# Kernel optimization log

Hardware: AMD Instinct MI355X
Metric: run time of the kernel (lower is better)

## Reference

```python
import jax, jax.numpy as jnp
import numpy as np

DN = ('NCHW', 'OIHW', 'NCHW')

def dw_conv(x, w, pad):
    # depthwise conv, w: [C,1,k,k], groups=C
    return jax.lax.conv_general_dilated(x, w, (1, 1), [(pad, pad), (pad, pad)],
                                         dimension_numbers=DN, feature_group_count=x.shape[1])

def pw_conv(x, w):
    # 1x1 pointwise conv, w: [Cout,Cin,1,1]
    return jax.lax.conv_general_dilated(x, w, (1, 1), 'VALID', dimension_numbers=DN)

def hardswish(x):
    return x * jnp.clip(x + 3.0, 0.0, 6.0) * (1.0 / 6.0)

def batchnorm(x, g, b, m, v, eps=1e-5):
    scale = (g / jnp.sqrt(v + eps))[None, :, None, None]
    return (x - m[None, :, None, None]) * scale + b[None, :, None, None]

def layernorm(x, g, b, eps=1e-5):
    mu = x.mean(-1, keepdims=True)
    var = x.var(-1, keepdims=True)
    return (x - mu) / jnp.sqrt(var + eps) * g + b

def setup_inputs() -> dict:
    key = jax.random.key(0)
    ks = jax.random.split(key, 16)
    B, C, H, W = 8, 256, 64, 64
    sd = 64   # seg_dim
    s = 0.05  # weight init scale
    inp = {
        'x':   jax.random.normal(ks[0], (B, C, H, W), jnp.float32),
        'seg': jax.random.normal(ks[1], (B, C, H, W), jnp.float32),
        'kv_w':   jax.random.normal(ks[2], (2 * C, C), jnp.float32) * s,
        'q_w':    jax.random.normal(ks[3], (C, C), jnp.float32) * s,
        'proj_w': jax.random.normal(ks[4], (C, C), jnp.float32) * s,
        'proj_b': jnp.zeros((C,), jnp.float32),
        'agg0_dw': jax.random.normal(ks[5], (3 * sd, 1, 3, 3), jnp.float32) * s,
        'agg0_pw': jax.random.normal(ks[6], (sd, 3 * sd, 1, 1), jnp.float32) * s,
        'ln_g': jnp.ones((sd,), jnp.float32), 'ln_b': jnp.zeros((sd,), jnp.float32),
        'agg1_dw': jax.random.normal(ks[7], (sd, 1, 3, 3), jnp.float32) * s,
        'agg1_pw': jax.random.normal(ks[8], (sd, sd, 1, 1), jnp.float32) * s,
        'bn1_g': jnp.ones((sd,), jnp.float32), 'bn1_b': jnp.zeros((sd,), jnp.float32),
        'bn1_m': jnp.zeros((sd,), jnp.float32), 'bn1_v': jnp.ones((sd,), jnp.float32),
        'agg2_dw': jax.random.normal(ks[9], (sd, 1, 5, 5), jnp.float32) * s,
        'agg2_pw': jax.random.normal(ks[10], (sd, sd, 1, 1), jnp.float32) * s,
        'bn2_g': jnp.ones((sd,), jnp.float32), 'bn2_b': jnp.zeros((sd,), jnp.float32),
        'bn2_m': jnp.zeros((sd,), jnp.float32), 'bn2_v': jnp.ones((sd,), jnp.float32),
        'agg3_dw': jax.random.normal(ks[11], (sd, 1, 7, 7), jnp.float32) * s,
        'agg3_pw': jax.random.normal(ks[12], (sd, sd, 1, 1), jnp.float32) * s,
        'bn3_g': jnp.ones((sd,), jnp.float32), 'bn3_b': jnp.zeros((sd,), jnp.float32),
        'bn3_m': jnp.zeros((sd,), jnp.float32), 'bn3_v': jnp.ones((sd,), jnp.float32),
        'crpe_w3': jax.random.normal(ks[13], (48, 1, 3, 3), jnp.float32) * s,
        'crpe_b3': jnp.zeros((48,), jnp.float32),
        'crpe_w5': jax.random.normal(ks[14], (72, 1, 5, 5), jnp.float32) * s,
        'crpe_b5': jnp.zeros((72,), jnp.float32),
        'crpe_w7': jax.random.normal(ks[15], (72, 1, 7, 7), jnp.float32) * s,
        'crpe_b7': jnp.zeros((72,), jnp.float32),
    }
    return inp

def reference(x, seg, kv_w, q_w, proj_w, proj_b, agg0_dw, agg0_pw, ln_g, ln_b,
              agg1_dw, agg1_pw, bn1_g, bn1_b, bn1_m, bn1_v,
              agg2_dw, agg2_pw, bn2_g, bn2_b, bn2_m, bn2_v,
              agg3_dw, agg3_pw, bn3_g, bn3_b, bn3_m, bn3_v,
              crpe_w3, crpe_b3, crpe_w5, crpe_b5, crpe_w7, crpe_b7):
    B, C, H, W = x.shape
    N = H * W
    num_heads = 8
    scale = (C // num_heads) ** -0.5  # head_dim = 32 -> 32^-0.5
    sd = C // 4                       # seg_dim = 64
    Ct = C // 4 * 3                   # trans_dim = 192
    Ch = Ct // num_heads              # 24

    # NOTE: faithful to torch: plain reshape of [B,C,H,W] -> [B,N,C] (no transpose)
    xf = x.reshape(B, N, C)
    sf = seg.reshape(B, N, C)

    kv = (xf @ kv_w.T).reshape(B, N, 2, C)
    kv = jnp.transpose(kv, (2, 0, 1, 3)).reshape(2 * B, N, C)
    q = sf @ q_w.T                                  # [B,N,C]
    qkv = jnp.concatenate([q, kv], axis=0)          # [3B,N,C]

    # ---- Aggregator ----
    xa = jnp.transpose(qkv, (0, 2, 1)).reshape(3 * B, C, H, W)
    c0, c1, c2, c3 = (xa[:, :sd], xa[:, sd:2 * sd], xa[:, 2 * sd:3 * sd], xa[:, 3 * sd:])
    # agg0 branch (local): regroup q/k/v copies into channels
    xl = c3.reshape(3, B, sd, H, W)
    xl = jnp.transpose(xl, (1, 0, 2, 3, 4)).reshape(B, 3 * sd, H, W)
    xl = pw_conv(dw_conv(xl, agg0_dw, 1), agg0_pw)  # [B,sd,H,W]
    xl = jnp.transpose(xl.reshape(B, sd, N), (0, 2, 1))
    x_agg0 = hardswish(layernorm(xl, ln_g, ln_b))   # [B,N,sd]

    x1 = hardswish(batchnorm(pw_conv(dw_conv(c0, agg1_dw, 1), agg1_pw), bn1_g, bn1_b, bn1_m, bn1_v))
    x2 = hardswish(batchnorm(pw_conv(dw_conv(c1, agg2_dw, 2), agg2_pw), bn2_g, bn2_b, bn2_m, bn2_v))
    x3 = hardswish(batchnorm(pw_conv(dw_conv(c2, agg3_dw, 3), agg3_pw), bn3_g, bn3_b, bn3_m, bn3_v))
    xc = jnp.concatenate([x1, x2, x3], axis=1)       # [3B,Ct,H,W]
    qkv_t = xc.reshape(3, B, num_heads, Ch, N)
    qkv_t = jnp.transpose(qkv_t, (0, 1, 2, 4, 3))    # [3,B,h,N,Ch]
    qh, kh, vh = qkv_t[0], qkv_t[1], qkv_t[2]

    # ---- linear attention: softmax over tokens on k, then k^T v ----
    k_sm = jax.nn.softmax(kh, axis=2)                       # softmax over N
    ktv = jnp.einsum('bhnk,bhnv->bhkv', k_sm, vh)           # [B,h,Ch,Ch]
    eff_att = jnp.einsum('bhnk,bhkv->bhnv', qh, ktv)        # [B,h,N,Ch]

    # ---- ConvRelPosEnc ----
    v_img = jnp.transpose(vh, (0, 1, 3, 2)).reshape(B, num_heads * Ch, H, W)
    s1, s2 = 2 * Ch, 2 * Ch + 3 * Ch   # channel splits [48,72,72]
    cv3 = dw_conv(v_img[:, :s1], crpe_w3, 1) + crpe_b3[None, :, None, None]
    cv5 = dw_conv(v_img[:, s1:s2], crpe_w5, 2) + crpe_b5[None, :, None, None]
    cv7 = dw_conv(v_img[:, s2:], crpe_w7, 3) + crpe_b7[None, :, None, None]
    conv_v = jnp.concatenate([cv3, cv5, cv7], axis=1)
    conv_v = jnp.transpose(conv_v.reshape(B, num_heads, Ch, N), (0, 1, 3, 2))  # [B,h,N,Ch]
    crpe = qh * conv_v

    out = scale * eff_att + crpe                     # [B,h,N,Ch]
    out = jnp.transpose(out, (0, 2, 1, 3)).reshape(B, N, Ct)
    out = jnp.concatenate([out, x_agg0], axis=-1)    # [B,N,C]
    out = out @ proj_w.T + proj_b
    return out
```

## Files before the change

### kernel.cpp

```cpp
#include <hip/hip_runtime.h>
#include <math.h>

#define DI __device__ __forceinline__

typedef unsigned short u16;
typedef __attribute__((ext_vector_type(8))) short bf16x8;
typedef __attribute__((ext_vector_type(4))) float f32x4;

static constexpr int Cc = 256;
static constexpr int Nn = 4096;

DI float hswish(float v) { return v * fminf(fmaxf(v + 3.f, 0.f), 6.f) * (1.f / 6.f); }

DI u16 f2b(float f) {
  union { float f; unsigned int u; } c; c.f = f;
  return (u16)((c.u + 0x7FFFu + ((c.u >> 16) & 1u)) >> 16);
}

typedef const __attribute__((address_space(1))) unsigned int* gas1_t;
typedef __attribute__((address_space(3))) unsigned int* las3_t;
DI void gld16(const void* g, void* l) {
  __builtin_amdgcn_global_load_lds((gas1_t)g, (las3_t)l, 16, 0, 0);
}

__global__ __launch_bounds__(256) void k_cvt(
    const float4* __restrict__ x, const float4* __restrict__ seg,
    const float4* __restrict__ kvw, const float4* __restrict__ qw,
    const float4* __restrict__ pw,
    ushort4* __restrict__ xb, ushort4* __restrict__ segb,
    ushort4* __restrict__ kvwb, ushort4* __restrict__ qwb,
    ushort4* __restrict__ pwb)
{
  const int total = 4259840;
  for (int i = blockIdx.x * 256 + threadIdx.x; i < total; i += gridDim.x * 256) {
    const float4* s; ushort4* d; int j;
    if (i < 2097152)      { s = x;   d = xb;   j = i; }
    else if (i < 4194304) { s = seg; d = segb; j = i - 2097152; }
    else if (i < 4227072) { s = kvw; d = kvwb; j = i - 4194304; }
    else if (i < 4243456) { s = qw;  d = qwb;  j = i - 4227072; }
    else                  { s = pw;  d = pwb;  j = i - 4243456; }
    float4 v = s[j];
    ushort4 o;
    o.x = f2b(v.x); o.y = f2b(v.y); o.z = f2b(v.z); o.w = f2b(v.w);
    d[j] = o;
  }
}

__global__ __launch_bounds__(256) void k_qkv(
    const u16* __restrict__ xb, const u16* __restrict__ segb,
    const u16* __restrict__ kvwb, const u16* __restrict__ qwb,
    float* __restrict__ qkv)
{
  __shared__ __align__(16) u16 As[2][4096];
  __shared__ __align__(16) u16 Bs[2][4096];
  const int t = threadIdx.x;
  const int lane = t & 63, wave = t >> 6;
  const int n0 = blockIdx.x * 128;
  const int c0 = blockIdx.y * 128;
  const int g  = blockIdx.z;
  const int grp = g >> 3, b = g & 7;
  const u16* __restrict__ In = (grp == 0 ? segb : xb) + (size_t)b * Nn * Cc;
  const u16* __restrict__ Wg = (grp == 0) ? qwb : (kvwb + (grp == 2 ? Cc * Cc : 0));

  const int rA = lane & 15;
  const int kA = (lane >> 4) * 8;
  const int s0 = wave * 2, s1 = wave * 2 + 1;

#define STAGE(buf, k0)                                                        \
  {                                                                           \
    gld16(Wg + (size_t)(c0 + s0 * 16 + rA) * Cc + (k0) + kA, &As[buf][s0 * 512]); \
    gld16(In + (size_t)(n0 + s0 * 16 + rA) * Cc + (k0) + kA, &Bs[buf][s0 * 512]); \
    gld16(Wg + (size_t)(c0 + s1 * 16 + rA) * Cc + (k0) + kA, &As[buf][s1 * 512]); \
    gld16(In + (size_t)(n0 + s1 * 16 + rA) * Cc + (k0) + kA, &Bs[buf][s1 * 512]); \
  }

  f32x4 acc[4][4];
#pragma unroll
  for (int m = 0; m < 4; ++m)
#pragma unroll
    for (int n = 0; n < 4; ++n) acc[m][n] = (f32x4){0.f, 0.f, 0.f, 0.f};

  const int asub = (wave >> 1) * 4;
  const int bsub = (wave & 1) * 4;

  STAGE(0, 0);
  for (int ks = 0; ks < 8; ++ks) {
    __syncthreads();
    if (ks < 7) STAGE((ks + 1) & 1, (ks + 1) * 32);
    const int cur = ks & 1;
    bf16x8 af[4], bfr[4];
#pragma unroll
    for (int m = 0; m < 4; ++m)
      af[m] = *(const bf16x8*)&As[cur][(asub + m) * 512 + lane * 8];
#pragma unroll
    for (int n = 0; n < 4; ++n)
      bfr[n] = *(const bf16x8*)&Bs[cur][(bsub + n) * 512 + lane * 8];
#pragma unroll
    for (int m = 0; m < 4; ++m)
#pragma unroll
      for (int n = 0; n < 4; ++n)
        acc[m][n] = __builtin_amdgcn_mfma_f32_16x16x32_bf16(af[m], bfr[n], acc[m][n], 0, 0, 0);
  }
#undef STAGE

  const int wc = (wave >> 1) * 64, wn = (wave & 1) * 64;
  const int row4 = (lane >> 4) * 4, col = lane & 15;
  float* __restrict__ op = qkv + (size_t)(g * Cc + c0 + wc) * Nn + n0 + wn;
#pragma unroll
  for (int m = 0; m < 4; ++m)
#pragma unroll
    for (int nn = 0; nn < 4; ++nn)
#pragma unroll
      for (int r = 0; r < 4; ++r)
        op[(size_t)(m * 16 + row4 + r) * Nn + nn * 16 + col] = acc[m][nn][r];
}

template <int KS>
DI void dw_plane(const float* __restrict__ sp, const float* __restrict__ wl,
                 float* __restrict__ dst, float bias, int t)
{
  constexpr int P = KS / 2;
  float wr[KS * KS];
#pragma unroll
  for (int i = 0; i < KS * KS; ++i) wr[i] = wl[i];
  const int x = t & 63;
  const int yb = (t >> 6) << 4;
  float acc[16];
#pragma unroll
  for (int i = 0; i < 16; ++i) acc[i] = bias;
#pragma unroll
  for (int r = 0; r < 16 + 2 * P; ++r) {
    float v[KS];
    const float* rp = sp + (yb + r + (3 - P)) * 70 + x + (3 - P);
#pragma unroll
    for (int dx = 0; dx < KS; ++dx) v[dx] = rp[dx];
#pragma unroll
    for (int dy = 0; dy < KS; ++dy) {
      const int yl = r - dy;
      if (yl >= 0 && yl < 16) {
        float s = acc[yl];
#pragma unroll
        for (int dx = 0; dx < KS; ++dx) s += wr[dy * KS + dx] * v[dx];
        acc[yl] = s;
      }
    }
  }
#pragma unroll
  for (int yl = 0; yl < 16; ++yl) dst[(yb + yl) * 64 + x] = acc[yl];
}

__global__ __launch_bounds__(256) void k_dw(
    const float* __restrict__ qkv,
    const float* __restrict__ a1w, const float* __restrict__ a2w,
    const float* __restrict__ a3w, const float* __restrict__ a0w,
    float* __restrict__ dwout, float* __restrict__ dwout0)
{
  __shared__ float sp[70 * 70];
  __shared__ float wl[49];
  const int t = threadIdx.x;
  const int p = blockIdx.x;
  const float* src; float* dst; const float* wsp; int ks;
  if (p < 4608) {
    int g = p / 192, c = p % 192, r = c >> 6;
    ks = 3 + 2 * r;
    wsp = (r == 0 ? a1w : (r == 1 ? a2w : a3w)) + (c & 63) * ks * ks;
    src = qkv + (size_t)(g * 256 + c) * Nn;
    dst = dwout + (size_t)p * Nn;
  } else {
    int q = p - 4608;
    int b = q / 192, j = q % 192;
    ks = 3;
    wsp = a0w + j * 9;
    src = qkv + (size_t)(((j >> 6) * 8 + b) * 256 + 192 + (j & 63)) * Nn;
    dst = dwout0 + (size_t)q * Nn;
  }
  for (int i = t; i < 4900; i += 256) sp[i] = 0.f;
  if (t < 49) wl[t] = (t < ks * ks) ? wsp[t] : 0.f;
  __syncthreads();
#pragma unroll
  for (int i = 0; i < 16; ++i) {
    int e = t + i * 256;
    sp[((e >> 6) + 3) * 70 + (e & 63) + 3] = src[e];
  }
  __syncthreads();
  if (ks == 3)      dw_plane<3>(sp, wl, dst, 0.f, t);
  else if (ks == 5) dw_plane<5>(sp, wl, dst, 0.f, t);
  else              dw_plane<7>(sp, wl, dst, 0.f, t);
}

__global__ __launch_bounds__(256) void k_crpe(
    const float* __restrict__ xc,
    const float* __restrict__ w3, const float* __restrict__ b3,
    const float* __restrict__ w5, const float* __restrict__ b5,
    const float* __restrict__ w7, const float* __restrict__ b7,
    float* __restrict__ conv_v)
{
  __shared__ float sp[70 * 70];
  __shared__ float wl[49];
  const int t = threadIdx.x;
  const int p = blockIdx.x;
  const int b = p / 192, ch = p % 192;
  const float* wsp; float bias; int ks;
  if (ch < 48)       { ks = 3; wsp = w3 + ch * 9;          bias = b3[ch]; }
  else if (ch < 120) { ks = 5; wsp = w5 + (ch - 48) * 25;  bias = b5[ch - 48]; }
  else               { ks = 7; wsp = w7 + (ch - 120) * 49; bias = b7[ch - 120]; }
  const float* src = xc + (size_t)((16 + b) * 192 + ch) * Nn;
  float* dst = conv_v + (size_t)p * Nn;
  for (int i = t; i < 4900; i += 256) sp[i] = 0.f;
  if (t < 49) wl[t] = (t < ks * ks) ? wsp[t] : 0.f;
  __syncthreads();
#pragma unroll
  for (int i = 0; i < 16; ++i) {
    int e = t + i * 256;
    sp[((e >> 6) + 3) * 70 + (e & 63) + 3] = src[e];
  }
  __syncthreads();
  if (ks == 3)      dw_plane<3>(sp, wl, dst, bias, t);
  else if (ks == 5) dw_plane<5>(sp, wl, dst, bias, t);
  else              dw_plane<7>(sp, wl, dst, bias, t);
}

__global__ __launch_bounds__(256) void k_pw_bn(
    const float* __restrict__ dwout,
    const float* __restrict__ w1, const float* __restrict__ w2, const float* __restrict__ w3,
    const float* __restrict__ g1, const float* __restrict__ be1, const float* __restrict__ m1, const float* __restrict__ v1,
    const float* __restrict__ g2, const float* __restrict__ be2, const float* __restrict__ m2, const float* __restrict__ v2,
    const float* __restrict__ g3, const float* __restrict__ be3, const float* __restrict__ m3, const float* __restrict__ v3,
    float* __restrict__ xc)
{
  __shared__ float Tl[64][128];
  __shared__ float Wt[64][64];
  const int t = threadIdx.x;
  const int n0 = blockIdx.x * 128;
  const int r = blockIdx.y;
  const int g = blockIdx.z;
  const float* Wp = (r == 0 ? w1 : (r == 1 ? w2 : w3));
  const float* bg = (r == 0 ? g1 : (r == 1 ? g2 : g3));
  const float* bb = (r == 0 ? be1 : (r == 1 ? be2 : be3));
  const float* bm = (r == 0 ? m1 : (r == 1 ? m2 : m3));
  const float* bv = (r == 0 ? v1 : (r == 1 ? v2 : v3));
  const size_t ibase = (size_t)(g * 192 + r * 64) * Nn + n0;
#pragma unroll
  for (int i = 0; i < 8; ++i) {
    int e = t + i * 256;
    int ci = e >> 5, nf = (e & 31) * 4;
    *(float4*)&Tl[ci][nf] = *(const float4*)(dwout + ibase + (size_t)ci * Nn + nf);
  }
#pragma unroll
  for (int i = 0; i < 16; ++i) {
    int e = t + i * 256;
    int co = e & 63, ci = e >> 6;
    Wt[ci][co] = Wp[co * 64 + ci];
  }
  __syncthreads();
  const int tn = (t & 15) * 4;
  const int tc = (t >> 4) * 4;
  float acc[4][8];
#pragma unroll
  for (int i = 0; i < 4; ++i)
#pragma unroll
    for (int j = 0; j < 8; ++j) acc[i][j] = 0.f;
#pragma unroll 8
  for (int ci = 0; ci < 64; ++ci) {
    const float4 i0 = *(const float4*)&Tl[ci][tn];
    const float4 i1 = *(const float4*)&Tl[ci][64 + tn];
    const float4 wv = *(const float4*)&Wt[ci][tc];
    const float iv[8] = {i0.x, i0.y, i0.z, i0.w, i1.x, i1.y, i1.z, i1.w};
    const float wa[4] = {wv.x, wv.y, wv.z, wv.w};
#pragma unroll
    for (int i = 0; i < 4; ++i)
#pragma unroll
      for (int j = 0; j < 8; ++j) acc[i][j] += wa[i] * iv[j];
  }
  const size_t obase = (size_t)(g * 192 + r * 64 + tc) * Nn + n0;
#pragma unroll
  for (int i = 0; i < 4; ++i) {
    int co = tc + i;
    float sc = bg[co] * rsqrtf(bv[co] + 1e-5f);
    float sh = bb[co] - bm[co] * sc;
    float4 o0, o1;
    o0.x = hswish(acc[i][0] * sc + sh); o0.y = hswish(acc[i][1] * sc + sh);
    o0.z = hswish(acc[i][2] * sc + sh); o0.w = hswish(acc[i][3] * sc + sh);
    o1.x = hswish(acc[i][4] * sc + sh); o1.y = hswish(acc[i][5] * sc + sh);
    o1.z = hswish(acc[i][6] * sc + sh); o1.w = hswish(acc[i][7] * sc + sh);
    *(float4*)(xc + obase + (size_t)i * Nn + tn) = o0;
    *(float4*)(xc + obase + (size_t)i * Nn + 64 + tn) = o1;
  }
}

__global__ __launch_bounds__(256) void k_pw_ln(
    const float* __restrict__ dwout0, const float* __restrict__ pw,
    const float* __restrict__ lng, const float* __restrict__ lnb,
    float* __restrict__ x_agg0)
{
  __shared__ float Tl[64][128];
  __shared__ float Wt[64][64];
  const int t = threadIdx.x;
  const int n0 = blockIdx.x * 128;
  const int b = blockIdx.y;
  const int tn = (t & 15) * 4;
  const int tc = (t >> 4) * 4;
  float acc[4][8];
#pragma unroll
  for (int i = 0; i < 4; ++i)
#pragma unroll
    for (int j = 0; j < 8; ++j) acc[i][j] = 0.f;

  for (int kc = 0; kc < 192; kc += 64) {
#pragma unroll
    for (int i = 0; i < 8; ++i) {
      int e = t + i * 256;
      int ci = e >> 5, nf = (e & 31) * 4;
      *(float4*)&Tl[ci][nf] =
          *(const float4*)(dwout0 + (size_t)(b * 192 + kc + ci) * Nn + n0 + nf);
    }
#pragma unroll
    for (int i = 0; i < 16; ++i) {
      int e = t + i * 256;
      int co = e & 63, ci = e >> 6;
      Wt[ci][co] = pw[co * 192 + kc + ci];
    }
    __syncthreads();
#pragma unroll 8
    for (int ci = 0; ci < 64; ++ci) {
      const float4 i0 = *(const float4*)&Tl[ci][tn];
      const float4 i1 = *(const float4*)&Tl[ci][64 + tn];
      const float4 wv = *(const float4*)&Wt[ci][tc];
      const float iv[8] = {i0.x, i0.y, i0.z, i0.w, i1.x, i1.y, i1.z, i1.w};
      const float wa[4] = {wv.x, wv.y, wv.z, wv.w};
#pragma unroll
      for (int i = 0; i < 4; ++i)
#pragma unroll
        for (int j = 0; j < 8; ++j) acc[i][j] += wa[i] * iv[j];
    }
    __syncthreads();
  }
  float* redS = &Tl[0][0];
  float* redQ = &Tl[0][0] + 2048;
  float* muA = &Tl[0][0] + 4096;
  float* isA = &Tl[0][0] + 4224;
#pragma unroll
  for (int j = 0; j < 8; ++j) {
    int nl = (j < 4) ? (tn + j) : (64 + tn + j - 4);
    float s = acc[0][j] + acc[1][j] + acc[2][j] + acc[3][j];
    float q = acc[0][j] * acc[0][j] + acc[1][j] * acc[1][j] +
              acc[2][j] * acc[2][j] + acc[3][j] * acc[3][j];
    redS[(t >> 4) * 128 + nl] = s;
    redQ[(t >> 4) * 128 + nl] = q;
  }
  __syncthreads();
  if (t < 128) {
    float s = 0.f, q = 0.f;
#pragma unroll
    for (int rr = 0; rr < 16; ++rr) { s += redS[rr * 128 + t]; q += redQ[rr * 128 + t]; }
    float mu = s * (1.f / 64.f);
    float var = q * (1.f / 64.f) - mu * mu;
    muA[t] = mu;
    isA[t] = rsqrtf(var + 1e-5f);
  }
  __syncthreads();
  float lg[4], lb[4];
#pragma unroll
  for (int i = 0; i < 4; ++i) { lg[i] = lng[tc + i]; lb[i] = lnb[tc + i]; }
#pragma unroll
  for (int j = 0; j < 8; ++j) {
    int nl = (j < 4) ? (tn + j) : (64 + tn + j - 4);
    float mu = muA[nl], is = isA[nl];
    float4 o;
    o.x = hswish((acc[0][j] - mu) * is * lg[0] + lb[0]);
    o.y = hswish((acc[1][j] - mu) * is * lg[1] + lb[1]);
    o.z = hswish((acc[2][j] - mu) * is * lg[2] + lb[2]);
    o.w = hswish((acc[3][j] - mu) * is * lg[3] + lb[3]);
    *(float4*)(x_agg0 + (size_t)((b << 12) + n0 + nl) * 64 + tc) = o;
  }
}

__global__ __launch_bounds__(256) void k_sm(const float* __restrict__ xc,
                                            float* __restrict__ ls)
{
  __shared__ float rA[4], rB[4];
  const int rho = blockIdx.x;
  const int b = rho / 192, rem = rho % 192;
  const float* row = xc + (size_t)((8 + b) * 192 + rem) * Nn;
  const int t = threadIdx.x;
  float v[16];
#pragma unroll
  for (int i = 0; i < 16; ++i) v[i] = row[t + i * 256];
  float m = v[0];
#pragma unroll
  for (int i = 1; i < 16; ++i) m = fmaxf(m, v[i]);
#pragma unroll
  for (int off = 32; off > 0; off >>= 1) m = fmaxf(m, __shfl_xor(m, off, 64));
  if ((t & 63) == 0) rA[t >> 6] = m;
  __syncthreads();
  m = fmaxf(fmaxf(rA[0], rA[1]), fmaxf(rA[2], rA[3]));
  float s = 0.f;
#pragma unroll
  for (int i = 0; i < 16; ++i) s += __expf(v[i] - m);
#pragma unroll
  for (int off = 32; off > 0; off >>= 1) s += __shfl_xor(s, off, 64);
  if ((t & 63) == 0) rB[t >> 6] = s;
  __syncthreads();
  if (t == 0) ls[rho] = m + __logf(rB[0] + rB[1] + rB[2] + rB[3]);
}

__global__ __launch_bounds__(576) void k_ktv(const float* __restrict__ xc,
                                             const float* __restrict__ ls,
                                             float* __restrict__ ktv)
{
  __shared__ float pb[24][65];
  __shared__ float vb[24][65];
  __shared__ float lsl[24];
  const int nc = blockIdx.x, h = blockIdx.y, b = blockIdx.z;
  const int t = threadIdx.x;
  if (t < 24) lsl[t] = ls[(b * 8 + h) * 24 + t];
  __syncthreads();
  const int kk = t / 24, vv = t % 24;
  const float* kbase = xc + (size_t)((8 + b) * 192 + h * 24) * Nn;
  const float* vbase = xc + (size_t)((16 + b) * 192 + h * 24) * Nn;
  const int nb0 = nc * 512;
  float accv = 0.f;
  for (int sub = 0; sub < 8; ++sub) {
    int nbase = nb0 + sub * 64;
    for (int e = t; e < 1536; e += 576) {
      int ch = e >> 6, n = e & 63;
      pb[ch][n] = __expf(kbase[(size_t)ch * Nn + nbase + n] - lsl[ch]);
      vb[ch][n] = vbase[(size_t)ch * Nn + nbase + n];
    }
    __syncthreads();
    float a = 0.f;
#pragma unroll 16
    for (int i = 0; i < 64; ++i) a += pb[kk][i] * vb[vv][i];
    accv += a;
    __syncthreads();
  }
  atomicAdd(&ktv[((b * 8 + h) * 24 + kk) * 24 + vv], accv);
}

__global__ __launch_bounds__(256) void k_cat(
    const float* __restrict__ xc, const float* __restrict__ conv_v,
    const float* __restrict__ ktv, const float* __restrict__ x_agg0,
    u16* __restrict__ catb)
{
  __shared__ float kt[4608];
  const int t = threadIdx.x;
  const int b = blockIdx.y;
  for (int e = t; e < 4608; e += 256) kt[e] = ktv[b * 4608 + e];
  __syncthreads();
  const int nl = t & 63;
  const int grp = t >> 6;
  const int n = blockIdx.x * 64 + nl;
  const float scale = 0.17677669529663687f;
#pragma unroll
  for (int hh = 0; hh < 2; ++hh) {
    const int h = grp * 2 + hh;
    const float* qb = xc + (size_t)(b * 192 + h * 24) * Nn + n;
    float q[24];
#pragma unroll
    for (int c = 0; c < 24; ++c) q[c] = qb[(size_t)c * Nn];
    float ev[24];
#pragma unroll
    for (int v = 0; v < 24; ++v) ev[v] = 0.f;
    const float* kth = kt + h * 576;
#pragma unroll
    for (int k = 0; k < 24; ++k) {
      const float qk = q[k];
#pragma unroll
      for (int v = 0; v < 24; ++v) ev[v] += qk * kth[k * 24 + v];
    }
    const float* cvb = conv_v + (size_t)(b * 192 + h * 24) * Nn + n;
    u16* ob = catb + ((size_t)(b * 4096 + n)) * 256 + h * 24;
#pragma unroll
    for (int v4 = 0; v4 < 6; ++v4) {
      ushort4 o;
      o.x = f2b(scale * ev[v4 * 4 + 0] + q[v4 * 4 + 0] * cvb[(size_t)(v4 * 4 + 0) * Nn]);
      o.y = f2b(scale * ev[v4 * 4 + 1] + q[v4 * 4 + 1] * cvb[(size_t)(v4 * 4 + 1) * Nn]);
      o.z = f2b(scale * ev[v4 * 4 + 2] + q[v4 * 4 + 2] * cvb[(size_t)(v4 * 4 + 2) * Nn]);
      o.w = f2b(scale * ev[v4 * 4 + 3] + q[v4 * 4 + 3] * cvb[(size_t)(v4 * 4 + 3) * Nn]);
      *(ushort4*)(ob + v4 * 4) = o;
    }
  }
  const float* xa = x_agg0 + ((size_t)(b * 4096 + blockIdx.x * 64)) * 64;
  u16* cb = catb + ((size_t)(b * 4096 + blockIdx.x * 64)) * 256 + 192;
  for (int e2 = t; e2 < 4096; e2 += 256) {
    int nn = e2 >> 6, cc = e2 & 63;
    cb[(size_t)nn * 256 + cc] = f2b(xa[(size_t)nn * 64 + cc]);
  }
}

__global__ __launch_bounds__(256) void k_proj(
    const u16* __restrict__ catb, const u16* __restrict__ pwb,
    const float* __restrict__ pb, float* __restrict__ out)
{
  __shared__ __align__(16) u16 As[2][4096];
  __shared__ __align__(16) u16 Bs[2][4096];
  const int t = threadIdx.x;
  const int lane = t & 63, wave = t >> 6;
  const int m0 = blockIdx.x * 128;
  const int c0 = blockIdx.y * 128;
  const int rA = lane & 15;
  const int kA = (lane >> 4) * 8;
  const int s0 = wave * 2, s1 = wave * 2 + 1;

#define STAGE(buf, k0)                                                        \
  {                                                                           \
    gld16(catb + (size_t)(m0 + s0 * 16 + rA) * 256 + (k0) + kA, &As[buf][s0 * 512]); \
    gld16(pwb  + (size_t)(c0 + s0 * 16 + rA) * 256 + (k0) + kA, &Bs[buf][s0 * 512]); \
    gld16(catb + (size_t)(m0 + s1 * 16 + rA) * 256 + (k0) + kA, &As[buf][s1 * 512]); \
    gld16(pwb  + (size_t)(c0 + s1 * 16 + rA) * 256 + (k0) + kA, &Bs[buf][s1 * 512]); \
  }

  f32x4 acc[4][4];
#pragma unroll
  for (int m = 0; m < 4; ++m)
#pragma unroll
    for (int n = 0; n < 4; ++n) acc[m][n] = (f32x4){0.f, 0.f, 0.f, 0.f};

  const int asub = (wave >> 1) * 4;
  const int bsub = (wave & 1) * 4;

  STAGE(0, 0);
  for (int ks = 0; ks < 8; ++ks) {
    __syncthreads();
    if (ks < 7) STAGE((ks + 1) & 1, (ks + 1) * 32);
    const int cur = ks & 1;
    bf16x8 af[4], bfr[4];
#pragma unroll
    for (int m = 0; m < 4; ++m)
      af[m] = *(const bf16x8*)&As[cur][(asub + m) * 512 + lane * 8];
#pragma unroll
    for (int n = 0; n < 4; ++n)
      bfr[n] = *(const bf16x8*)&Bs[cur][(bsub + n) * 512 + lane * 8];
#pragma unroll
    for (int m = 0; m < 4; ++m)
#pragma unroll
      for (int n = 0; n < 4; ++n)
        acc[m][n] = __builtin_amdgcn_mfma_f32_16x16x32_bf16(af[m], bfr[n], acc[m][n], 0, 0, 0);
  }
#undef STAGE

  const int wm = (wave >> 1) * 64, wn = (wave & 1) * 64;
  const int row4 = (lane >> 4) * 4, col = lane & 15;
  float pbv[4];
#pragma unroll
  for (int nn = 0; nn < 4; ++nn) pbv[nn] = pb[c0 + wn + nn * 16 + col];
  float* __restrict__ op = out + (size_t)(m0 + wm) * 256 + c0 + wn;
#pragma unroll
  for (int mi = 0; mi < 4; ++mi)
#pragma unroll
    for (int nn = 0; nn < 4; ++nn)
#pragma unroll
      for (int r = 0; r < 4; ++r)
        op[(size_t)(mi * 16 + row4 + r) * 256 + nn * 16 + col] = acc[mi][nn][r] + pbv[nn];
}

extern "C" void kernel_launch(void* const* d_in, const int* in_sizes, int n_in,
                              void* d_out, int out_size, void* d_ws, size_t ws_size,
                              hipStream_t stream)
{
  const float* x       = (const float*)d_in[0];
  const float* seg     = (const float*)d_in[1];
  const float* kv_w    = (const float*)d_in[2];
  const float* q_w     = (const float*)d_in[3];
  const float* proj_w  = (const float*)d_in[4];
  const float* proj_b  = (const float*)d_in[5];
  const float* agg0_dw = (const float*)d_in[6];
  const float* agg0_pw = (const float*)d_in[7];
  const float* ln_g    = (const float*)d_in[8];
  const float* ln_b    = (const float*)d_in[9];
  const float* agg1_dw = (const float*)d_in[10];
  const float* agg1_pw = (const float*)d_in[11];
  const float* bn1_g   = (const float*)d_in[12];
  const float* bn1_b   = (const float*)d_in[13];
  const float* bn1_m   = (const float*)d_in[14];
  const float* bn1_v   = (const float*)d_in[15];
  const float* agg2_dw = (const float*)d_in[16];
  const float* agg2_pw = (const float*)d_in[17];
  const float* bn2_g   = (const float*)d_in[18];
  const float* bn2_b   = (const float*)d_in[19];
  const float* bn2_m   = (const float*)d_in[20];
  const float* bn2_v   = (const float*)d_in[21];
  const float* agg3_dw = (const float*)d_in[22];
  const float* agg3_pw = (const float*)d_in[23];
  const float* bn3_g   = (const float*)d_in[24];
  const float* bn3_b   = (const float*)d_in[25];
  const float* bn3_m   = (const float*)d_in[26];
  const float* bn3_v   = (const float*)d_in[27];
  const float* crpe_w3 = (const float*)d_in[28];
  const float* crpe_b3 = (const float*)d_in[29];
  const float* crpe_w5 = (const float*)d_in[30];
  const float* crpe_b5 = (const float*)d_in[31];
  const float* crpe_w7 = (const float*)d_in[32];
  const float* crpe_b7 = (const float*)d_in[33];

  float* ws = (float*)d_ws;
  float* qkv    = ws;
  float* xcbuf  = ws;
  float* dwout  = ws + 25165824;
  float* conv_v = dwout;
  u16*   xb     = (u16*)(ws + 25165824);
  u16*   segb   = (u16*)(ws + 29360128);
  u16*   kvwb   = (u16*)(ws + 33554432);
  u16*   qwb    = (u16*)(ws + 33619968);
  float* dwout0 = ws + 44040192;
  u16*   catb   = (u16*)(ws + 44040192);
  float* x_agg0 = ws + 50331648;
  float* ls     = ws + 52428800;
  float* ktv    = ws + 52430336;
  u16*   pwb    = (u16*)(ws + 52467200);
  float* out    = (float*)d_out;

  hipMemsetAsync(ktv, 0, 36864 * sizeof(float), stream);

  k_cvt<<<dim3(1024), 256, 0, stream>>>(
      (const float4*)x, (const float4*)seg, (const float4*)kv_w,
      (const float4*)q_w, (const float4*)proj_w,
      (ushort4*)xb, (ushort4*)segb, (ushort4*)kvwb, (ushort4*)qwb, (ushort4*)pwb);
  k_qkv<<<dim3(32, 2, 24), 256, 0, stream>>>(xb, segb, kvwb, qwb, qkv);
  k_dw<<<dim3(6144), 256, 0, stream>>>(qkv, agg1_dw, agg2_dw, agg3_dw, agg0_dw,
                                       dwout, dwout0);
  k_pw_bn<<<dim3(32, 3, 24), 256, 0, stream>>>(
      dwout, agg1_pw, agg2_pw, agg3_pw,
      bn1_g, bn1_b, bn1_m, bn1_v,
      bn2_g, bn2_b, bn2_m, bn2_v,
      bn3_g, bn3_b, bn3_m, bn3_v, xcbuf);
  k_pw_ln<<<dim3(32, 8), 256, 0, stream>>>(dwout0, agg0_pw, ln_g, ln_b, x_agg0);
  k_sm<<<dim3(1536), 256, 0, stream>>>(xcbuf, ls);
  k_ktv<<<dim3(8, 8, 8), 576, 0, stream>>>(xcbuf, ls, ktv);
  k_crpe<<<dim3(1536), 256, 0, stream>>>(xcbuf, crpe_w3, crpe_b3, crpe_w5,
                                         crpe_b5, crpe_w7, crpe_b7, conv_v);
  k_cat<<<dim3(64, 8), 256, 0, stream>>>(xcbuf, conv_v, ktv, x_agg0, catb);
  k_proj<<<dim3(256, 2), 256, 0, stream>>>(catb, pwb, proj_b, out);
}
```

Baseline: 400.2 us.

## Store intermediates in bf16, fuse input conversion into GEMMs, use MFMA for pointwise convs

Removes the separate fp32-to-bf16 conversion kernel. The QKV and projection GEMMs now load fp32 inputs and convert them in registers before writing to LDS. All intermediate activations (qkv, depthwise outputs, xc, conv_v, x_agg0) are stored as bf16 instead of fp32, roughly halving intermediate memory traffic. The pointwise BN and LN convolutions switch from scalar FMA to bf16 MFMA, and depthwise staging zeroes only the halo with a padded stride. The cost is lower-precision intermediates and losing the async global_load_lds path for the converted operands.

```diff
diff --git a/kernel.cpp b/kernel.cpp
--- a/kernel.cpp
+++ b/kernel.cpp
@@ -1,10 +1,10 @@
 #include <hip/hip_runtime.h>
-#include <math.h>
 
 #define DI __device__ __forceinline__
 
 typedef unsigned short u16;
 typedef __attribute__((ext_vector_type(8))) short bf16x8;
+typedef __attribute__((ext_vector_type(8))) unsigned short u16x8;
 typedef __attribute__((ext_vector_type(4))) float f32x4;
 
 static constexpr int Cc = 256;
@@ -15,6 +15,15 @@
 DI u16 f2b(float f) {
   union { float f; unsigned int u; } c; c.f = f;
   return (u16)((c.u + 0x7FFFu + ((c.u >> 16) & 1u)) >> 16);
+}
+DI float b2f(u16 v) {
+  union { unsigned int u; float f; } c; c.u = ((unsigned int)v) << 16; return c.f;
+}
+DI u16x8 pack8(float4 a, float4 b) {
+  u16x8 r;
+  r[0] = f2b(a.x); r[1] = f2b(a.y); r[2] = f2b(a.z); r[3] = f2b(a.w);
+  r[4] = f2b(b.x); r[5] = f2b(b.y); r[6] = f2b(b.z); r[7] = f2b(b.w);
+  return r;
 }
 
 typedef const __attribute__((address_space(1))) unsigned int* gas1_t;
@@ -23,33 +32,10 @@
   __builtin_amdgcn_global_load_lds((gas1_t)g, (las3_t)l, 16, 0, 0);
 }
 
-__global__ __launch_bounds__(256) void k_cvt(
-    const float4* __restrict__ x, const float4* __restrict__ seg,
-    const float4* __restrict__ kvw, const float4* __restrict__ qw,
-    const float4* __restrict__ pw,
-    ushort4* __restrict__ xb, ushort4* __restrict__ segb,
-    ushort4* __restrict__ kvwb, ushort4* __restrict__ qwb,
-    ushort4* __restrict__ pwb)
-{
-  const int total = 4259840;
-  for (int i = blockIdx.x * 256 + threadIdx.x; i < total; i += gridDim.x * 256) {
-    const float4* s; ushort4* d; int j;
-    if (i < 2097152)      { s = x;   d = xb;   j = i; }
-    else if (i < 4194304) { s = seg; d = segb; j = i - 2097152; }
-    else if (i < 4227072) { s = kvw; d = kvwb; j = i - 4194304; }
-    else if (i < 4243456) { s = qw;  d = qwb;  j = i - 4227072; }
-    else                  { s = pw;  d = pwb;  j = i - 4243456; }
-    float4 v = s[j];
-    ushort4 o;
-    o.x = f2b(v.x); o.y = f2b(v.y); o.z = f2b(v.z); o.w = f2b(v.w);
-    d[j] = o;
-  }
-}
-
 __global__ __launch_bounds__(256) void k_qkv(
-    const u16* __restrict__ xb, const u16* __restrict__ segb,
-    const u16* __restrict__ kvwb, const u16* __restrict__ qwb,
-    float* __restrict__ qkv)
+    const float* __restrict__ x, const float* __restrict__ seg,
+    const float* __restrict__ kv_w, const float* __restrict__ q_w,
+    u16* __restrict__ qkv)
 {
   __shared__ __align__(16) u16 As[2][4096];
   __shared__ __align__(16) u16 Bs[2][4096];
@@ -59,19 +45,27 @@
   const int c0 = blockIdx.y * 128;
   const int g  = blockIdx.z;
   const int grp = g >> 3, b = g & 7;
-  const u16* __restrict__ In = (grp == 0 ? segb : xb) + (size_t)b * Nn * Cc;
-  const u16* __restrict__ Wg = (grp == 0) ? qwb : (kvwb + (grp == 2 ? Cc * Cc : 0));
+  const float* __restrict__ In = (grp == 0 ? seg : x) + (size_t)b * Nn * Cc;
+  const float* __restrict__ Wg = (grp == 0) ? q_w : (kv_w + (grp == 2 ? Cc * Cc : 0));
 
   const int rA = lane & 15;
   const int kA = (lane >> 4) * 8;
   const int s0 = wave * 2, s1 = wave * 2 + 1;
 
-#define STAGE(buf, k0)                                                        \
+#define STG(buf, k0)                                                          \
   {                                                                           \
-    gld16(Wg + (size_t)(c0 + s0 * 16 + rA) * Cc + (k0) + kA, &As[buf][s0 * 512]); \
-    gld16(In + (size_t)(n0 + s0 * 16 + rA) * Cc + (k0) + kA, &Bs[buf][s0 * 512]); \
-    gld16(Wg + (size_t)(c0 + s1 * 16 + rA) * Cc + (k0) + kA, &As[buf][s1 * 512]); \
-    gld16(In + (size_t)(n0 + s1 * 16 + rA) * Cc + (k0) + kA, &Bs[buf][s1 * 512]); \
+    const float* ap0 = Wg + (size_t)(c0 + s0 * 16 + rA) * Cc + (k0) + kA;     \
+    const float* ap1 = Wg + (size_t)(c0 + s1 * 16 + rA) * Cc + (k0) + kA;     \
+    const float* bp0 = In + (size_t)(n0 + s0 * 16 + rA) * Cc + (k0) + kA;     \
+    const float* bp1 = In + (size_t)(n0 + s1 * 16 + rA) * Cc + (k0) + kA;     \
+    float4 a0 = *(const float4*)ap0, a1 = *(const float4*)(ap0 + 4);          \
+    float4 a2 = *(const float4*)ap1, a3 = *(const float4*)(ap1 + 4);          \
+    float4 b0 = *(const float4*)bp0, b1 = *(const float4*)(bp0 + 4);          \
+    float4 b2 = *(const float4*)bp1, b3 = *(const float4*)(bp1 + 4);          \
+    *(u16x8*)&As[buf][s0 * 512 + lane * 8] = pack8(a0, a1);                   \
+    *(u16x8*)&As[buf][s1 * 512 + lane * 8] = pack8(a2, a3);                   \
+    *(u16x8*)&Bs[buf][s0 * 512 + lane * 8] = pack8(b0, b1);                   \
+    *(u16x8*)&Bs[buf][s1 * 512 + lane * 8] = pack8(b2, b3);                   \
   }
 
   f32x4 acc[4][4];
@@ -83,10 +77,10 @@
   const int asub = (wave >> 1) * 4;
   const int bsub = (wave & 1) * 4;
 
-  STAGE(0, 0);
+  STG(0, 0);
   for (int ks = 0; ks < 8; ++ks) {
     __syncthreads();
-    if (ks < 7) STAGE((ks + 1) & 1, (ks + 1) * 32);
+    if (ks < 7) STG((ks + 1) & 1, (ks + 1) * 32);
     const int cur = ks & 1;
     bf16x8 af[4], bfr[4];
 #pragma unroll
@@ -101,23 +95,23 @@
       for (int n = 0; n < 4; ++n)
         acc[m][n] = __builtin_amdgcn_mfma_f32_16x16x32_bf16(af[m], bfr[n], acc[m][n], 0, 0, 0);
   }
-#undef STAGE
+#undef STG
 
   const int wc = (wave >> 1) * 64, wn = (wave & 1) * 64;
   const int row4 = (lane >> 4) * 4, col = lane & 15;
-  float* __restrict__ op = qkv + (size_t)(g * Cc + c0 + wc) * Nn + n0 + wn;
+  u16* __restrict__ op = qkv + (size_t)(g * Cc + c0 + wc) * Nn + n0 + wn;
 #pragma unroll
   for (int m = 0; m < 4; ++m)
 #pragma unroll
     for (int nn = 0; nn < 4; ++nn)
 #pragma unroll
       for (int r = 0; r < 4; ++r)
-        op[(size_t)(m * 16 + row4 + r) * Nn + nn * 16 + col] = acc[m][nn][r];
+        op[(size_t)(m * 16 + row4 + r) * Nn + nn * 16 + col] = f2b(acc[m][nn][r]);
 }
 
 template <int KS>
 DI void dw_plane(const float* __restrict__ sp, const float* __restrict__ wl,
-                 float* __restrict__ dst, float bias, int t)
+                 u16* __restrict__ dst, float bias, int t)
 {
   constexpr int P = KS / 2;
   float wr[KS * KS];
@@ -131,7 +125,7 @@
 #pragma unroll
   for (int r = 0; r < 16 + 2 * P; ++r) {
     float v[KS];
-    const float* rp = sp + (yb + r + (3 - P)) * 70 + x + (3 - P);
+    const float* rp = sp + (yb + r + (3 - P)) * 72 + x + (4 - P);
 #pragma unroll
     for (int dx = 0; dx < KS; ++dx) v[dx] = rp[dx];
 #pragma unroll
@@ -146,20 +140,46 @@
     }
   }
 #pragma unroll
-  for (int yl = 0; yl < 16; ++yl) dst[(yb + yl) * 64 + x] = acc[yl];
+  for (int yl = 0; yl < 16; ++yl) dst[(yb + yl) * 64 + x] = f2b(acc[yl]);
+}
+
+DI void dw_stage(const u16* __restrict__ src, float* __restrict__ sp, int t)
+{
+  for (int i = t; i < 944; i += 256) {
+    if (i < 432) {
+      int r6 = i / 72, cl = i - r6 * 72;
+      int row = (r6 < 3) ? r6 : 64 + r6;
+      sp[row * 72 + cl] = 0.f;
+    } else {
+      int i2 = i - 432;
+      int row = 3 + (i2 >> 3), k = i2 & 7;
+      int cl = (k < 4) ? k : 64 + k;
+      sp[row * 72 + cl] = 0.f;
+    }
+  }
+#pragma unroll
+  for (int i = 0; i < 2; ++i) {
+    int u = t + i * 256;
+    int row = u >> 3, c8 = (u & 7) * 8;
+    u16x8 v = *(const u16x8*)(src + row * 64 + c8);
+    float4 f0 = make_float4(b2f(v[0]), b2f(v[1]), b2f(v[2]), b2f(v[3]));
+    float4 f1 = make_float4(b2f(v[4]), b2f(v[5]), b2f(v[6]), b2f(v[7]));
+    *(float4*)&sp[(row + 3) * 72 + 4 + c8] = f0;
+    *(float4*)&sp[(row + 3) * 72 + 8 + c8] = f1;
+  }
 }
 
 __global__ __launch_bounds__(256) void k_dw(
-    const float* __restrict__ qkv,
+    const u16* __restrict__ qkv,
     const float* __restrict__ a1w, const float* __restrict__ a2w,
     const float* __restrict__ a3w, const float* __restrict__ a0w,
-    float* __restrict__ dwout, float* __restrict__ dwout0)
-{
-  __shared__ float sp[70 * 70];
+    u16* __restrict__ dwout, u16* __restrict__ dwout0)
+{
+  __shared__ float sp[70 * 72];
   __shared__ float wl[49];
   const int t = threadIdx.x;
   const int p = blockIdx.x;
-  const float* src; float* dst; const float* wsp; int ks;
+  const u16* src; u16* dst; const float* wsp; int ks;
   if (p < 4608) {
     int g = p / 192, c = p % 192, r = c >> 6;
     ks = 3 + 2 * r;
@@ -174,14 +194,8 @@
     src = qkv + (size_t)(((j >> 6) * 8 + b) * 256 + 192 + (j & 63)) * Nn;
     dst = dwout0 + (size_t)q * Nn;
   }
-  for (int i = t; i < 4900; i += 256) sp[i] = 0.f;
   if (t < 49) wl[t] = (t < ks * ks) ? wsp[t] : 0.f;
-  __syncthreads();
-#pragma unroll
-  for (int i = 0; i < 16; ++i) {
-    int e = t + i * 256;
-    sp[((e >> 6) + 3) * 70 + (e & 63) + 3] = src[e];
-  }
+  dw_stage(src, sp, t);
   __syncthreads();
   if (ks == 3)      dw_plane<3>(sp, wl, dst, 0.f, t);
   else if (ks == 5) dw_plane<5>(sp, wl, dst, 0.f, t);
@@ -189,13 +203,13 @@
 }
 
 __global__ __launch_bounds__(256) void k_crpe(
-    const float* __restrict__ xc,
+    const u16* __restrict__ xc,
     const float* __restrict__ w3, const float* __restrict__ b3,
     const float* __restrict__ w5, const float* __restrict__ b5,
     const float* __restrict__ w7, const float* __restrict__ b7,
-    float* __restrict__ conv_v)
-{
-  __shared__ float sp[70 * 70];
+    u16* __restrict__ conv_v)
+{
+  __shared__ float sp[70 * 72];
   __shared__ float wl[49];
   const int t = threadIdx.x;
   const int p = blockIdx.x;
@@ -204,16 +218,10 @@
   if (ch < 48)       { ks = 3; wsp = w3 + ch * 9;          bias = b3[ch]; }
   else if (ch < 120) { ks = 5; wsp = w5 + (ch - 48) * 25;  bias = b5[ch - 48]; }
   else               { ks = 7; wsp = w7 + (ch - 120) * 49; bias = b7[ch - 120]; }
-  const float* src = xc + (size_t)((16 + b) * 192 + ch) * Nn;
-  float* dst = conv_v + (size_t)p * Nn;
-  for (int i = t; i < 4900; i += 256) sp[i] = 0.f;
+  const u16* src = xc + (size_t)((16 + b) * 192 + ch) * Nn;
+  u16* dst = conv_v + (size_t)p * Nn;
   if (t < 49) wl[t] = (t < ks * ks) ? wsp[t] : 0.f;
-  __syncthreads();
-#pragma unroll
-  for (int i = 0; i < 16; ++i) {
-    int e = t + i * 256;
-    sp[((e >> 6) + 3) * 70 + (e & 63) + 3] = src[e];
-  }
+  dw_stage(src, sp, t);
   __syncthreads();
   if (ks == 3)      dw_plane<3>(sp, wl, dst, bias, t);
   else if (ks == 5) dw_plane<5>(sp, wl, dst, bias, t);
@@ -221,16 +229,19 @@
 }
 
 __global__ __launch_bounds__(256) void k_pw_bn(
-    const float* __restrict__ dwout,
+    const u16* __restrict__ dwout,
     const float* __restrict__ w1, const float* __restrict__ w2, const float* __restrict__ w3,
     const float* __restrict__ g1, const float* __restrict__ be1, const float* __restrict__ m1, const float* __restrict__ v1,
     const float* __restrict__ g2, const float* __restrict__ be2, const float* __restrict__ m2, const float* __restrict__ v2,
     const float* __restrict__ g3, const float* __restrict__ be3, const float* __restrict__ m3, const float* __restrict__ v3,
-    float* __restrict__ xc)
-{
-  __shared__ float Tl[64][128];
-  __shared__ float Wt[64][64];
-  const int t = threadIdx.x;
+    u16* __restrict__ xc)
+{
+  constexpr int S2 = 134;
+  __shared__ u16 Dl[64 * S2];
+  __shared__ __align__(16) u16 Wt[64 * 72];
+  __shared__ float scA[64], shA[64];
+  const int t = threadIdx.x;
+  const int lane = t & 63, wave = t >> 6;
   const int n0 = blockIdx.x * 128;
   const int r = blockIdx.y;
   const int g = blockIdx.z;
@@ -239,153 +250,180 @@
   const float* bb = (r == 0 ? be1 : (r == 1 ? be2 : be3));
   const float* bm = (r == 0 ? m1 : (r == 1 ? m2 : m3));
   const float* bv = (r == 0 ? v1 : (r == 1 ? v2 : v3));
-  const size_t ibase = (size_t)(g * 192 + r * 64) * Nn + n0;
-#pragma unroll
-  for (int i = 0; i < 8; ++i) {
-    int e = t + i * 256;
-    int ci = e >> 5, nf = (e & 31) * 4;
-    *(float4*)&Tl[ci][nf] = *(const float4*)(dwout + ibase + (size_t)ci * Nn + nf);
-  }
-#pragma unroll
-  for (int i = 0; i < 16; ++i) {
-    int e = t + i * 256;
-    int co = e & 63, ci = e >> 6;
-    Wt[ci][co] = Wp[co * 64 + ci];
+
+  {
+    int co = t >> 2, ci0 = (t & 3) * 16;
+    const float* wp = Wp + co * 64 + ci0;
+    float4 w0 = *(const float4*)wp,       wq = *(const float4*)(wp + 4);
+    float4 w2_ = *(const float4*)(wp + 8), w3_ = *(const float4*)(wp + 12);
+    *(u16x8*)&Wt[co * 72 + ci0] = pack8(w0, wq);
+    *(u16x8*)&Wt[co * 72 + ci0 + 8] = pack8(w2_, w3_);
+  }
+  if (t < 64) {
+    float sc = bg[t] * rsqrtf(bv[t] + 1e-5f);
+    scA[t] = sc; shA[t] = bb[t] - bm[t] * sc;
+  }
+  const u16* dbase = dwout + (size_t)(g * 192 + r * 64) * Nn + n0;
+#pragma unroll
+  for (int i2 = 0; i2 < 4; ++i2) {
+    int u = t + i2 * 256;
+    int ci = u >> 4, nu = u & 15;
+    u16x8 v = *(const u16x8*)(dbase + (size_t)ci * Nn + nu * 8);
+    union { u16x8 v; unsigned int w[4]; } cc; cc.v = v;
+    int base = ci * S2 + nu * 8;
+#pragma unroll
+    for (int w = 0; w < 4; ++w) *(unsigned int*)&Dl[base + 2 * w] = cc.w[w];
   }
   __syncthreads();
-  const int tn = (t & 15) * 4;
-  const int tc = (t >> 4) * 4;
-  float acc[4][8];
-#pragma unroll
-  for (int i = 0; i < 4; ++i)
-#pragma unroll
-    for (int j = 0; j < 8; ++j) acc[i][j] = 0.f;
-#pragma unroll 8
-  for (int ci = 0; ci < 64; ++ci) {
-    const float4 i0 = *(const float4*)&Tl[ci][tn];
-    const float4 i1 = *(const float4*)&Tl[ci][64 + tn];
-    const float4 wv = *(const float4*)&Wt[ci][tc];
-    const float iv[8] = {i0.x, i0.y, i0.z, i0.w, i1.x, i1.y, i1.z, i1.w};
-    const float wa[4] = {wv.x, wv.y, wv.z, wv.w};
-#pragma unroll
-    for (int i = 0; i < 4; ++i)
-#pragma unroll
-      for (int j = 0; j < 8; ++j) acc[i][j] += wa[i] * iv[j];
-  }
-  const size_t obase = (size_t)(g * 192 + r * 64 + tc) * Nn + n0;
-#pragma unroll
-  for (int i = 0; i < 4; ++i) {
-    int co = tc + i;
-    float sc = bg[co] * rsqrtf(bv[co] + 1e-5f);
-    float sh = bb[co] - bm[co] * sc;
-    float4 o0, o1;
-    o0.x = hswish(acc[i][0] * sc + sh); o0.y = hswish(acc[i][1] * sc + sh);
-    o0.z = hswish(acc[i][2] * sc + sh); o0.w = hswish(acc[i][3] * sc + sh);
-    o1.x = hswish(acc[i][4] * sc + sh); o1.y = hswish(acc[i][5] * sc + sh);
-    o1.z = hswish(acc[i][6] * sc + sh); o1.w = hswish(acc[i][7] * sc + sh);
-    *(float4*)(xc + obase + (size_t)i * Nn + tn) = o0;
-    *(float4*)(xc + obase + (size_t)i * Nn + 64 + tn) = o1;
-  }
+
+  f32x4 acc[4][2];
+#pragma unroll
+  for (int m = 0; m < 4; ++m)
+#pragma unroll
+    for (int n = 0; n < 2; ++n) acc[m][n] = (f32x4){0.f, 0.f, 0.f, 0.f};
+
+#pragma unroll
+  for (int ks = 0; ks < 2; ++ks) {
+    const int kbase = ks * 32 + (lane >> 4) * 8;
+    bf16x8 af[4];
+#pragma unroll
+    for (int m = 0; m < 4; ++m)
+      af[m] = *(const bf16x8*)&Wt[(m * 16 + (lane & 15)) * 72 + kbase];
+#pragma unroll
+    for (int nl = 0; nl < 2; ++nl) {
+      const int ncol = (wave * 2 + nl) * 16 + (lane & 15);
+      bf16x8 bf;
+#pragma unroll
+      for (int j = 0; j < 8; ++j) bf[j] = (short)Dl[(kbase + j) * S2 + ncol];
+#pragma unroll
+      for (int m = 0; m < 4; ++m)
+        acc[m][nl] = __builtin_amdgcn_mfma_f32_16x16x32_bf16(af[m], bf, acc[m][nl], 0, 0, 0);
+    }
+  }
+
+  const int row4 = (lane >> 4) * 4, col = lane & 15;
+#pragma unroll
+  for (int m = 0; m < 4; ++m)
+#pragma unroll
+    for (int nl = 0; nl < 2; ++nl) {
+      int nn = (wave * 2 + nl) * 16 + col;
+      u16* op = xc + (size_t)(g * 192 + r * 64 + m * 16 + row4) * Nn + n0 + nn;
+#pragma unroll
+      for (int rr = 0; rr < 4; ++rr) {
+        int co = m * 16 + row4 + rr;
+        float v = acc[m][nl][rr] * scA[co] + shA[co];
+        op[(size_t)rr * Nn] = f2b(hswish(v));
+      }
+    }
 }
 
 __global__ __launch_bounds__(256) void k_pw_ln(
-    const float* __restrict__ dwout0, const float* __restrict__ pw,
+    const u16* __restrict__ dwout0, const float* __restrict__ pw,
     const float* __restrict__ lng, const float* __restrict__ lnb,
-    float* __restrict__ x_agg0)
-{
-  __shared__ float Tl[64][128];
-  __shared__ float Wt[64][64];
-  const int t = threadIdx.x;
+    u16* __restrict__ x_agg0)
+{
+  constexpr int S2 = 134;
+  __shared__ u16 Dl[64 * S2];
+  __shared__ __align__(16) u16 Wt[64 * 200];
+  __shared__ float lgA[64], lbA[64];
+  const int t = threadIdx.x;
+  const int lane = t & 63, wave = t >> 6;
   const int n0 = blockIdx.x * 128;
   const int b = blockIdx.y;
-  const int tn = (t & 15) * 4;
-  const int tc = (t >> 4) * 4;
-  float acc[4][8];
-#pragma unroll
-  for (int i = 0; i < 4; ++i)
-#pragma unroll
-    for (int j = 0; j < 8; ++j) acc[i][j] = 0.f;
+
+#pragma unroll
+  for (int i = 0; i < 12; ++i) {
+    int u = t + i * 256;
+    int co = u / 48, rem = u - co * 48;
+    float4 w = *(const float4*)(pw + co * 192 + rem * 4);
+    ushort4 o; o.x = f2b(w.x); o.y = f2b(w.y); o.z = f2b(w.z); o.w = f2b(w.w);
+    *(ushort4*)&Wt[co * 200 + rem * 4] = o;
+  }
+  if (t < 64) { lgA[t] = lng[t]; lbA[t] = lnb[t]; }
+
+  f32x4 acc[4][2];
+#pragma unroll
+  for (int m = 0; m < 4; ++m)
+#pragma unroll
+    for (int n = 0; n < 2; ++n) acc[m][n] = (f32x4){0.f, 0.f, 0.f, 0.f};
 
   for (int kc = 0; kc < 192; kc += 64) {
-#pragma unroll
-    for (int i = 0; i < 8; ++i) {
-      int e = t + i * 256;
-      int ci = e >> 5, nf = (e & 31) * 4;
-      *(float4*)&Tl[ci][nf] =
-          *(const float4*)(dwout0 + (size_t)(b * 192 + kc + ci) * Nn + n0 + nf);
-    }
-#pragma unroll
-    for (int i = 0; i < 16; ++i) {
-      int e = t + i * 256;
-      int co = e & 63, ci = e >> 6;
-      Wt[ci][co] = pw[co * 192 + kc + ci];
+    if (kc) __syncthreads();
+    const u16* dbase = dwout0 + (size_t)(b * 192 + kc) * Nn + n0;
+#pragma unroll
+    for (int i2 = 0; i2 < 4; ++i2) {
+      int u = t + i2 * 256;
+      int ci = u >> 4, nu = u & 15;
+      u16x8 v = *(const u16x8*)(dbase + (size_t)ci * Nn + nu * 8);
+      union { u16x8 v; unsigned int w[4]; } cc; cc.v = v;
+      int base = ci * S2 + nu * 8;
+#pragma unroll
+      for (int w = 0; w < 4; ++w) *(unsigned int*)&Dl[base + 2 * w] = cc.w[w];
     }
     __syncthreads();
-#pragma unroll 8
-    for (int ci = 0; ci < 64; ++ci) {
-      const float4 i0 = *(const float4*)&Tl[ci][tn];
-      const float4 i1 = *(const float4*)&Tl[ci][64 + tn];
-      const float4 wv = *(const float4*)&Wt[ci][tc];
-      const float iv[8] = {i0.x, i0.y, i0.z, i0.w, i1.x, i1.y, i1.z, i1.w};
-      const float wa[4] = {wv.x, wv.y, wv.z, wv.w};
-#pragma unroll
-      for (int i = 0; i < 4; ++i)
-#pragma unroll
-        for (int j = 0; j < 8; ++j) acc[i][j] += wa[i] * iv[j];
-    }
-    __syncthreads();
-  }
-  float* redS = &Tl[0][0];
-  float* redQ = &Tl[0][0] + 2048;
-  float* muA = &Tl[0][0] + 4096;
-  float* isA = &Tl[0][0] + 4224;
-#pragma unroll
-  for (int j = 0; j < 8; ++j) {
-    int nl = (j < 4) ? (tn + j) : (64 + tn + j - 4);
-    float s = acc[0][j] + acc[1][j] + acc[2][j] + acc[3][j];
-    float q = acc[0][j] * acc[0][j] + acc[1][j] * acc[1][j] +
-              acc[2][j] * acc[2][j] + acc[3][j] * acc[3][j];
-    redS[(t >> 4) * 128 + nl] = s;
-    redQ[(t >> 4) * 128 + nl] = q;
-  }
-  __syncthreads();
-  if (t < 128) {
+#pragma unroll
+    for (int ks = 0; ks < 2; ++ks) {
+      const int kbase = ks * 32 + (lane >> 4) * 8;
+      bf16x8 af[4];
+#pragma unroll
+      for (int m = 0; m < 4; ++m)
+        af[m] = *(const bf16x8*)&Wt[(m * 16 + (lane & 15)) * 200 + kc + kbase];
+#pragma unroll
+      for (int nl = 0; nl < 2; ++nl) {
+        const int ncol = (wave * 2 + nl) * 16 + (lane & 15);
+        bf16x8 bf;
+#pragma unroll
+        for (int j = 0; j < 8; ++j) bf[j] = (short)Dl[(kbase + j) * S2 + ncol];
+#pragma unroll
+        for (int m = 0; m < 4; ++m)
+          acc[m][nl] = __builtin_amdgcn_mfma_f32_16x16x32_bf16(af[m], bf, acc[m][nl], 0, 0, 0);
+      }
+    }
+  }
+
+  const int row4 = (lane >> 4) * 4, col = lane & 15;
+#pragma unroll
+  for (int nl = 0; nl < 2; ++nl) {
     float s = 0.f, q = 0.f;
 #pragma unroll
-    for (int rr = 0; rr < 16; ++rr) { s += redS[rr * 128 + t]; q += redQ[rr * 128 + t]; }
+    for (int m = 0; m < 4; ++m)
+#pragma unroll
+      for (int rr = 0; rr < 4; ++rr) {
+        float v = acc[m][nl][rr];
+        s += v; q += v * v;
+      }
+    s += __shfl_xor(s, 16, 64); q += __shfl_xor(q, 16, 64);
+    s += __shfl_xor(s, 32, 64); q += __shfl_xor(q, 32, 64);
     float mu = s * (1.f / 64.f);
     float var = q * (1.f / 64.f) - mu * mu;
-    muA[t] = mu;
-    isA[t] = rsqrtf(var + 1e-5f);
-  }
-  __syncthreads();
-  float lg[4], lb[4];
-#pragma unroll
-  for (int i = 0; i < 4; ++i) { lg[i] = lng[tc + i]; lb[i] = lnb[tc + i]; }
-#pragma unroll
-  for (int j = 0; j < 8; ++j) {
-    int nl = (j < 4) ? (tn + j) : (64 + tn + j - 4);
-    float mu = muA[nl], is = isA[nl];
-    float4 o;
-    o.x = hswish((acc[0][j] - mu) * is * lg[0] + lb[0]);
-    o.y = hswish((acc[1][j] - mu) * is * lg[1] + lb[1]);
-    o.z = hswish((acc[2][j] - mu) * is * lg[2] + lb[2]);
-    o.w = hswish((acc[3][j] - mu) * is * lg[3] + lb[3]);
-    *(float4*)(x_agg0 + (size_t)((b << 12) + n0 + nl) * 64 + tc) = o;
-  }
-}
-
-__global__ __launch_bounds__(256) void k_sm(const float* __restrict__ xc,
+    float is = rsqrtf(var + 1e-5f);
+    int nn = (wave * 2 + nl) * 16 + col;
+    u16* op = x_agg0 + (size_t)((b << 12) + n0 + nn) * 64;
+#pragma unroll
+    for (int m = 0; m < 4; ++m) {
+      ushort4 o;
+#pragma unroll
+      for (int rr = 0; rr < 4; ++rr) {
+        int co = m * 16 + row4 + rr;
+        float v = (acc[m][nl][rr] - mu) * is * lgA[co] + lbA[co];
+        ((u16*)&o)[rr] = f2b(hswish(v));
+      }
+      *(ushort4*)&op[m * 16 + row4] = o;
+    }
+  }
+}
+
+__global__ __launch_bounds__(256) void k_sm(const u16* __restrict__ xc,
                                             float* __restrict__ ls)
 {
   __shared__ float rA[4], rB[4];
   const int rho = blockIdx.x;
   const int b = rho / 192, rem = rho % 192;
-  const float* row = xc + (size_t)((8 + b) * 192 + rem) * Nn;
+  const u16* row = xc + (size_t)((8 + b) * 192 + rem) * Nn;
   const int t = threadIdx.x;
   float v[16];
 #pragma unroll
-  for (int i = 0; i < 16; ++i) v[i] = row[t + i * 256];
+  for (int i = 0; i < 16; ++i) v[i] = b2f(row[t + i * 256]);
   float m = v[0];
 #pragma unroll
   for (int i = 1; i < 16; ++i) m = fmaxf(m, v[i]);
@@ -404,7 +442,7 @@
   if (t == 0) ls[rho] = m + __logf(rB[0] + rB[1] + rB[2] + rB[3]);
 }
 
-__global__ __launch_bounds__(576) void k_ktv(const float* __restrict__ xc,
+__global__ __launch_bounds__(576) void k_ktv(const u16* __restrict__ xc,
                                              const float* __restrict__ ls,
                                              float* __restrict__ ktv)
 {
@@ -416,16 +454,16 @@
   if (t < 24) lsl[t] = ls[(b * 8 + h) * 24 + t];
   __syncthreads();
   const int kk = t / 24, vv = t % 24;
-  const float* kbase = xc + (size_t)((8 + b) * 192 + h * 24) * Nn;
-  const float* vbase = xc + (size_t)((16 + b) * 192 + h * 24) * Nn;
+  const u16* kbase = xc + (size_t)((8 + b) * 192 + h * 24) * Nn;
+  const u16* vbase = xc + (size_t)((16 + b) * 192 + h * 24) * Nn;
   const int nb0 = nc * 512;
   float accv = 0.f;
   for (int sub = 0; sub < 8; ++sub) {
     int nbase = nb0 + sub * 64;
     for (int e = t; e < 1536; e += 576) {
       int ch = e >> 6, n = e & 63;
-      pb[ch][n] = __expf(kbase[(size_t)ch * Nn + nbase + n] - lsl[ch]);
-      vb[ch][n] = vbase[(size_t)ch * Nn + nbase + n];
+      pb[ch][n] = __expf(b2f(kbase[(size_t)ch * Nn + nbase + n]) - lsl[ch]);
+      vb[ch][n] = b2f(vbase[(size_t)ch * Nn + nbase + n]);
     }
     __syncthreads();
     float a = 0.f;
@@ -438,8 +476,8 @@
 }
 
 __global__ __launch_bounds__(256) void k_cat(
-    const float* __restrict__ xc, const float* __restrict__ conv_v,
-    const float* __restrict__ ktv, const float* __restrict__ x_agg0,
+    const u16* __restrict__ xc, const u16* __restrict__ conv_v,
+    const float* __restrict__ ktv, const u16* __restrict__ x_agg0,
     u16* __restrict__ catb)
 {
   __shared__ float kt[4608];
@@ -454,10 +492,10 @@
 #pragma unroll
   for (int hh = 0; hh < 2; ++hh) {
     const int h = grp * 2 + hh;
-    const float* qb = xc + (size_t)(b * 192 + h * 24) * Nn + n;
+    const u16* qb = xc + (size_t)(b * 192 + h * 24) * Nn + n;
     float q[24];
 #pragma unroll
-    for (int c = 0; c < 24; ++c) q[c] = qb[(size_t)c * Nn];
+    for (int c = 0; c < 24; ++c) q[c] = b2f(qb[(size_t)c * Nn]);
     float ev[24];
 #pragma unroll
     for (int v = 0; v < 24; ++v) ev[v] = 0.f;
@@ -468,28 +506,28 @@
 #pragma unroll
       for (int v = 0; v < 24; ++v) ev[v] += qk * kth[k * 24 + v];
     }
-    const float* cvb = conv_v + (size_t)(b * 192 + h * 24) * Nn + n;
+    const u16* cvb = conv_v + (size_t)(b * 192 + h * 24) * Nn + n;
     u16* ob = catb + ((size_t)(b * 4096 + n)) * 256 + h * 24;
 #pragma unroll
     for (int v4 = 0; v4 < 6; ++v4) {
       ushort4 o;
-      o.x = f2b(scale * ev[v4 * 4 + 0] + q[v4 * 4 + 0] * cvb[(size_t)(v4 * 4 + 0) * Nn]);
-      o.y = f2b(scale * ev[v4 * 4 + 1] + q[v4 * 4 + 1] * cvb[(size_t)(v4 * 4 + 1) * Nn]);
-      o.z = f2b(scale * ev[v4 * 4 + 2] + q[v4 * 4 + 2] * cvb[(size_t)(v4 * 4 + 2) * Nn]);
-      o.w = f2b(scale * ev[v4 * 4 + 3] + q[v4 * 4 + 3] * cvb[(size_t)(v4 * 4 + 3) * Nn]);
+      o.x = f2b(scale * ev[v4 * 4 + 0] + q[v4 * 4 + 0] * b2f(cvb[(size_t)(v4 * 4 + 0) * Nn]));
+      o.y = f2b(scale * ev[v4 * 4 + 1] + q[v4 * 4 + 1] * b2f(cvb[(size_t)(v4 * 4 + 1) * Nn]));
+      o.z = f2b(scale * ev[v4 * 4 + 2] + q[v4 * 4 + 2] * b2f(cvb[(size_t)(v4 * 4 + 2) * Nn]));
+      o.w = f2b(scale * ev[v4 * 4 + 3] + q[v4 * 4 + 3] * b2f(cvb[(size_t)(v4 * 4 + 3) * Nn]));
       *(ushort4*)(ob + v4 * 4) = o;
     }
   }
-  const float* xa = x_agg0 + ((size_t)(b * 4096 + blockIdx.x * 64)) * 64;
+  const u16* xa = x_agg0 + ((size_t)(b * 4096 + blockIdx.x * 64)) * 64;
   u16* cb = catb + ((size_t)(b * 4096 + blockIdx.x * 64)) * 256 + 192;
   for (int e2 = t; e2 < 4096; e2 += 256) {
     int nn = e2 >> 6, cc = e2 & 63;
-    cb[(size_t)nn * 256 + cc] = f2b(xa[(size_t)nn * 64 + cc]);
+    cb[(size_t)nn * 256 + cc] = xa[(size_t)nn * 64 + cc];
   }
 }
 
 __global__ __launch_bounds__(256) void k_proj(
-    const u16* __restrict__ catb, const u16* __restrict__ pwb,
+    const u16* __restrict__ catb, const float* __restrict__ pwf,
     const float* __restrict__ pb, float* __restrict__ out)
 {
   __shared__ __align__(16) u16 As[2][4096];
@@ -502,12 +540,16 @@
   const int kA = (lane >> 4) * 8;
   const int s0 = wave * 2, s1 = wave * 2 + 1;
 
-#define STAGE(buf, k0)                                                        \
+#define STG(buf, k0)                                                          \
   {                                                                           \
     gld16(catb + (size_t)(m0 + s0 * 16 + rA) * 256 + (k0) + kA, &As[buf][s0 * 512]); \
-    gld16(pwb  + (size_t)(c0 + s0 * 16 + rA) * 256 + (k0) + kA, &Bs[buf][s0 * 512]); \
     gld16(catb + (size_t)(m0 + s1 * 16 + rA) * 256 + (k0) + kA, &As[buf][s1 * 512]); \
-    gld16(pwb  + (size_t)(c0 + s1 * 16 + rA) * 256 + (k0) + kA, &Bs[buf][s1 * 512]); \
+    const float* bp0 = pwf + (size_t)(c0 + s0 * 16 + rA) * 256 + (k0) + kA;   \
+    const float* bp1 = pwf + (size_t)(c0 + s1 * 16 + rA) * 256 + (k0) + kA;   \
+    float4 b0 = *(const float4*)bp0, b1 = *(const float4*)(bp0 + 4);          \
+    float4 b2 = *(const float4*)bp1, b3 = *(const float4*)(bp1 + 4);          \
+    *(u16x8*)&Bs[buf][s0 * 512 + lane * 8] = pack8(b0, b1);                   \
+    *(u16x8*)&Bs[buf][s1 * 512 + lane * 8] = pack8(b2, b3);                   \
   }
 
   f32x4 acc[4][4];
@@ -519,10 +561,10 @@
   const int asub = (wave >> 1) * 4;
   const int bsub = (wave & 1) * 4;
 
-  STAGE(0, 0);
+  STG(0, 0);
   for (int ks = 0; ks < 8; ++ks) {
     __syncthreads();
-    if (ks < 7) STAGE((ks + 1) & 1, (ks + 1) * 32);
+    if (ks < 7) STG((ks + 1) & 1, (ks + 1) * 32);
     const int cur = ks & 1;
     bf16x8 af[4], bfr[4];
 #pragma unroll
@@ -537,7 +579,7 @@
       for (int n = 0; n < 4; ++n)
         acc[m][n] = __builtin_amdgcn_mfma_f32_16x16x32_bf16(af[m], bfr[n], acc[m][n], 0, 0, 0);
   }
-#undef STAGE
+#undef STG
 
   const int wm = (wave >> 1) * 64, wn = (wave & 1) * 64;
   const int row4 = (lane >> 4) * 4, col = lane & 15;
@@ -594,41 +636,32 @@
   const float* crpe_b7 = (const float*)d_in[33];
 
   float* ws = (float*)d_ws;
-  float* qkv    = ws;
-  float* xcbuf  = ws;
-  float* dwout  = ws + 25165824;
-  float* conv_v = dwout;
-  u16*   xb     = (u16*)(ws + 25165824);
-  u16*   segb   = (u16*)(ws + 29360128);
-  u16*   kvwb   = (u16*)(ws + 33554432);
-  u16*   qwb    = (u16*)(ws + 33619968);
-  float* dwout0 = ws + 44040192;
-  u16*   catb   = (u16*)(ws + 44040192);
-  float* x_agg0 = ws + 50331648;
-  float* ls     = ws + 52428800;
-  float* ktv    = ws + 52430336;
-  u16*   pwb    = (u16*)(ws + 52467200);
+  u16*   qkv_b  = (u16*)(ws);
+  u16*   dwout  = (u16*)(ws + 12582912);
+  u16*   dwout0 = (u16*)(ws + 22020096);
+  u16*   xc_b   = (u16*)(ws + 25165824);
+  u16*   conv_v = (u16*)(ws + 37748736);
+  u16*   x_agg0 = (u16*)(ws + 40894464);
+  float* ls     = ws + 41943040;
+  float* ktv    = ws + 41944576;
+  u16*   catb   = (u16*)(ws + 41981440);
   float* out    = (float*)d_out;
 
   hipMemsetAsync(ktv, 0, 36864 * sizeof(float), stream);
 
-  k_cvt<<<dim3(1024), 256, 0, stream>>>(
-      (const float4*)x, (const float4*)seg, (const float4*)kv_w,
-      (const float4*)q_w, (const float4*)proj_w,
-      (ushort4*)xb, (ushort4*)segb, (ushort4*)kvwb, (ushort4*)qwb, (ushort4*)pwb);
-  k_qkv<<<dim3(32, 2, 24), 256, 0, stream>>>(xb, segb, kvwb, qwb, qkv);
-  k_dw<<<dim3(6144), 256, 0, stream>>>(qkv, agg1_dw, agg2_dw, agg3_dw, agg0_dw,
+  k_qkv<<<dim3(32, 2, 24), 256, 0, stream>>>(x, seg, kv_w, q_w, qkv_b);
+  k_dw<<<dim3(6144), 256, 0, stream>>>(qkv_b, agg1_dw, agg2_dw, agg3_dw, agg0_dw,
                                        dwout, dwout0);
   k_pw_bn<<<dim3(32, 3, 24), 256, 0, stream>>>(
       dwout, agg1_pw, agg2_pw, agg3_pw,
       bn1_g, bn1_b, bn1_m, bn1_v,
       bn2_g, bn2_b, bn2_m, bn2_v,
-      bn3_g, bn3_b, bn3_m, bn3_v, xcbuf);
+      bn3_g, bn3_b, bn3_m, bn3_v, xc_b);
   k_pw_ln<<<dim3(32, 8), 256, 0, stream>>>(dwout0, agg0_pw, ln_g, ln_b, x_agg0);
-  k_sm<<<dim3(1536), 256, 0, stream>>>(xcbuf, ls);
-  k_ktv<<<dim3(8, 8, 8), 576, 0, stream>>>(xcbuf, ls, ktv);
-  k_crpe<<<dim3(1536), 256, 0, stream>>>(xcbuf, crpe_w3, crpe_b3, crpe_w5,
+  k_sm<<<dim3(1536), 256, 0, stream>>>(xc_b, ls);
+  k_ktv<<<dim3(8, 8, 8), 576, 0, stream>>>(xc_b, ls, ktv);
+  k_crpe<<<dim3(1536), 256, 0, stream>>>(xc_b, crpe_w3, crpe_b3, crpe_w5,
                                          crpe_b5, crpe_w7, crpe_b7, conv_v);
-  k_cat<<<dim3(64, 8), 256, 0, stream>>>(xcbuf, conv_v, ktv, x_agg0, catb);
-  k_proj<<<dim3(256, 2), 256, 0, stream>>>(catb, pwb, proj_b, out);
-}
+  k_cat<<<dim3(64, 8), 256, 0, stream>>>(xc_b, conv_v, ktv, x_agg0, catb);
+  k_proj<<<dim3(256, 2), 256, 0, stream>>>(catb, proj_w, proj_b, out);
+}
```

Result: faster. 363.0 us (-9.3%).
